# Optimization experiments

Hardware: AMD Instinct MI355X
Metric: run time of the kernel (lower is better)

The kernel has to match this reference:

```python
import jax, jax.numpy as jnp
import numpy as np

T_LATENCY = 2  # refractory latency (timesteps), from init_kwargs
FS_SCALE = 10.0  # FastSigmoid surrogate scale


@jax.custom_vjp
def fast_sigmoid_spike(u):
    return (u > 0).astype(u.dtype)

def _fs_fwd(u):
    return fast_sigmoid_spike(u), u

def _fs_bwd(u, g):
    return (g / (FS_SCALE * jnp.abs(u) + 1.0) ** 2,)

fast_sigmoid_spike.defvjp(_fs_fwd, _fs_bwd)


def setup_inputs() -> dict:
    key = jax.random.key(0)
    k1, k2, k3, k4 = jax.random.split(key, 4)
    B, N, T = 64, 1024, 512
    x = jax.random.normal(k1, (B, N, T), dtype=jnp.float32)
    beta = jax.random.uniform(k2, (N,), jnp.float32, 0.3, 0.95)   # leak
    p = jax.random.uniform(k3, (N,), jnp.float32, 0.5, 0.95)      # adaptation decay
    b = jax.random.uniform(k4, (N,), jnp.float32, 0.5, 1.5)       # adaptation strength
    return {"x": x, "beta": beta, "p": p, "b": b}


def reference(x, beta, p, b):
    # clamped effective params (matches torch @property accessors)
    beta_c = jnp.clip(beta, 0.001, 0.999)
    p_c = jnp.clip(jnp.abs(p), 0.0, 0.999)
    b_c = jnp.clip(jnp.abs(b), 0.001, 1.0)

    B, N, T = x.shape
    xt = jnp.moveaxis(x, 2, 0)  # [T, B, N]

    def step(carry, x_t):
        mem, spikes, refac, a, v_th = carry
        # spike-triggered refractory reset, then mask input during refractory window
        refac = jnp.where(spikes > 0, 0.0, refac)
        ic = jnp.where(refac < T_LATENCY, 0.0, x_t)
        refac = refac + 1.0
        # leaky integration
        new_mem = mem * beta_c + ic
        s = fast_sigmoid_spike(new_mem - v_th)
        # reset-by-subtraction-to-zero with detached spikes (detach_spike_grad=True)
        mem = new_mem * (1.0 - jax.lax.stop_gradient(s))
        # adaptive threshold
        a = p_c * a + s
        v_th = 1.0 + b_c * a
        return (mem, s, refac, a, v_th), s

    z = jnp.zeros((B, N), x.dtype)
    init = (z, z, jnp.full((B, N), float(T_LATENCY), x.dtype), z,
            jnp.ones((B, N), x.dtype))
    _, spikes_seq = jax.lax.scan(step, init, xt)  # [T, B, N]
    return jnp.moveaxis(spikes_seq, 0, 2)  # [B, N, T]
```

## Files before the change

### kernel.cpp

```cpp
#include <hip/hip_runtime.h>

#pragma clang fp contract(off)

#define ROWS    64
#define T_LEN   512
#define CHUNK   64
#define NCHUNK  (T_LEN / CHUNK)
#define STRIDE  (CHUNK + 1)
#define NV      16
#define NPARAM  1024

typedef float f4_nt __attribute__((ext_vector_type(4)));

#define BARRIER() asm volatile("s_waitcnt lgkmcnt(0)\n\ts_barrier" ::: "memory")

__global__ __launch_bounds__(192) void snn_fwd(
    const float* __restrict__ x,
    const float* __restrict__ beta,
    const float* __restrict__ p,
    const float* __restrict__ bparam,
    float* __restrict__ out)
{
    __shared__ float inbuf[2][ROWS * STRIDE];
    __shared__ float outbuf[ROWS * STRIDE];

    const int tid     = threadIdx.x;
    const int wid     = tid >> 6;
    const int lane    = tid & 63;
    const int rowBase = blockIdx.x * ROWS;

    const float4* __restrict__ xv = (const float4*)x;
    float4* __restrict__ ov       = (float4*)out;

    const int t16 = lane & 15;
    const int r4  = lane >> 4;
    const int gq  = (rowBase + r4) * (T_LEN / 4) + t16;
    const int lf  = r4 * STRIDE + t16 * 4;

    float mem = 0.0f, refac = 2.0f, a = 0.0f, vth = 1.0f, ps = 0.0f;
    float beta_c = 0.f, p_c = 0.f, b_c = 0.f;
    const int cb = lane * STRIDE;

    if (wid == 0) {
        const int n = (rowBase + lane) & (NPARAM - 1);
        beta_c = fminf(fmaxf(beta[n], 0.001f), 0.999f);
        p_c    = fminf(fabsf(p[n]), 0.999f);
        b_c    = fminf(fmaxf(fabsf(bparam[n]), 0.001f), 1.0f);
    }

    auto step = [&](float xt) -> float {
        refac = (ps > 0.0f) ? 0.0f : refac;
        const float ic = (refac < 2.0f) ? 0.0f : xt;
        refac += 1.0f;
        const float nm   = __fadd_rn(__fmul_rn(mem, beta_c), ic);
        const float diff = __fsub_rn(nm, vth);
        const float s    = (diff > 0.0f) ? 1.0f : 0.0f;
        mem = (diff > 0.0f) ? 0.0f : nm;
        a   = __fadd_rn(__fmul_rn(p_c, a), s);
        vth = __fadd_rn(1.0f, __fmul_rn(b_c, a));
        ps  = s;
        return s;
    };

    float4 ld[NV];

    auto loadChunk = [&](int k) {
        const int base = gq + k * NV;
        #pragma unroll
        for (int it = 0; it < NV; ++it)
            ld[it] = xv[base + it * 4 * (T_LEN / 4)];
    };
    auto stage = [&](int buf) {
        #pragma unroll
        for (int it = 0; it < NV; ++it) {
            const int o = lf + it * 4 * STRIDE;
            inbuf[buf][o + 0] = ld[it].x;
            inbuf[buf][o + 1] = ld[it].y;
            inbuf[buf][o + 2] = ld[it].z;
            inbuf[buf][o + 3] = ld[it].w;
        }
    };
    auto drain = [&](int k) {
        const int base = gq + k * NV;
        #pragma unroll
        for (int it = 0; it < NV; ++it) {
            const int o = lf + it * 4 * STRIDE;
            float4 sv;
            sv.x = outbuf[o + 0];
            sv.y = outbuf[o + 1];
            sv.z = outbuf[o + 2];
            sv.w = outbuf[o + 3];
            __builtin_nontemporal_store(
                *reinterpret_cast<f4_nt*>(&sv),
                reinterpret_cast<f4_nt*>(&ov[base + it * 4 * (T_LEN / 4)]));
        }
    };

    if (wid == 1) {
        loadChunk(0);
        stage(0);
        loadChunk(1);
    }
    BARRIER();

    #pragma unroll 1
    for (int k = 0; k < NCHUNK; ++k) {
        const int cur = k & 1;
        float sv[CHUNK];
        if (wid == 0) {
            #pragma unroll
            for (int t = 0; t < CHUNK; ++t)
                sv[t] = step(inbuf[cur][cb + t]);
        } else if (wid == 1) {
            if (k + 1 < NCHUNK) stage(cur ^ 1);
            if (k + 2 < NCHUNK) loadChunk(k + 2);
        } else {
            if (k > 0) drain(k - 1);
        }
        BARRIER();
        if (wid == 0) {
            #pragma unroll
            for (int t = 0; t < CHUNK; ++t)
                outbuf[cb + t] = sv[t];
        }
        BARRIER();
    }
    if (wid == 2) drain(NCHUNK - 1);
}

extern "C" void kernel_launch(void* const* d_in, const int* in_sizes, int n_in,
                              void* d_out, int out_size, void* d_ws, size_t ws_size,
                              hipStream_t stream) {
    const float* x    = (const float*)d_in[0];
    const float* beta = (const float*)d_in[1];
    const float* p    = (const float*)d_in[2];
    const float* b    = (const float*)d_in[3];
    float* out        = (float*)d_out;

    const int BN = 64 * 1024;
    snn_fwd<<<dim3(BN / ROWS), dim3(192), 0, stream>>>(x, beta, p, b, out);
}
```

Baseline: 241.5 us.

## Compute spikes in place in double-buffered XOR-swizzled LDS with two I/O waves

The compute wave now writes spikes back over its input slot instead of into a separate output buffer, which removes the second barrier per chunk. The chunk doubles to 128 timesteps, halving the number of loop iterations and barriers. Padded rows are replaced by an XOR swizzle to avoid LDS bank conflicts. Both helper waves now split the load, stage and drain work for 32 rows each, and each drains the previous results before restaging the buffer. The cost is higher register pressure, since 128 steps are fully unrolled and each lane now holds the full NV float4 loads, and occupancy may drop with 64 KB of LDS per block.

```diff
diff --git a/kernel.cpp b/kernel.cpp
--- a/kernel.cpp
+++ b/kernel.cpp
@@ -4,11 +4,11 @@
 
 #define ROWS    64
 #define T_LEN   512
-#define CHUNK   64
+#define CHUNK   128
 #define NCHUNK  (T_LEN / CHUNK)
-#define STRIDE  (CHUNK + 1)
 #define NV      16
 #define NPARAM  1024
+#define BUF_FLOATS (ROWS * CHUNK)
 
 typedef float f4_nt __attribute__((ext_vector_type(4)));
 
@@ -21,8 +21,7 @@
     const float* __restrict__ bparam,
     float* __restrict__ out)
 {
-    __shared__ float inbuf[2][ROWS * STRIDE];
-    __shared__ float outbuf[ROWS * STRIDE];
+    __shared__ float smem[2][BUF_FLOATS];
 
     const int tid     = threadIdx.x;
     const int wid     = tid >> 6;
@@ -32,14 +31,15 @@
     const float4* __restrict__ xv = (const float4*)x;
     float4* __restrict__ ov       = (float4*)out;
 
-    const int t16 = lane & 15;
-    const int r4  = lane >> 4;
-    const int gq  = (rowBase + r4) * (T_LEN / 4) + t16;
-    const int lf  = r4 * STRIDE + t16 * 4;
+    const int t32 = lane & 31;
+    const int r2  = lane >> 5;
+    const int rw  = (wid > 0 ? (wid - 1) * 32 : 0) + r2;
+    const int gq  = (rowBase + rw) * (T_LEN / 4) + t32;
 
     float mem = 0.0f, refac = 2.0f, a = 0.0f, vth = 1.0f, ps = 0.0f;
     float beta_c = 0.f, p_c = 0.f, b_c = 0.f;
-    const int cb = lane * STRIDE;
+    const int crow = lane * CHUNK;
+    const int cxm  = lane & 31;
 
     if (wid == 0) {
         const int n = (rowBase + lane) & (NPARAM - 1);
@@ -65,67 +65,70 @@
     float4 ld[NV];
 
     auto loadChunk = [&](int k) {
-        const int base = gq + k * NV;
+        const int base = gq + k * (CHUNK / 4);
         #pragma unroll
         for (int it = 0; it < NV; ++it)
-            ld[it] = xv[base + it * 4 * (T_LEN / 4)];
+            ld[it] = xv[base + it * 2 * (T_LEN / 4)];
     };
-    auto stage = [&](int buf) {
+    auto stage = [&](float* buf) {
         #pragma unroll
         for (int it = 0; it < NV; ++it) {
-            const int o = lf + it * 4 * STRIDE;
-            inbuf[buf][o + 0] = ld[it].x;
-            inbuf[buf][o + 1] = ld[it].y;
-            inbuf[buf][o + 2] = ld[it].z;
-            inbuf[buf][o + 3] = ld[it].w;
+            const int row = rw + 2 * it;
+            const int o   = row * CHUNK;
+            const int xm  = row & 31;
+            const int c0  = t32 * 4;
+            buf[o + ((c0 + 0) ^ xm)] = ld[it].x;
+            buf[o + ((c0 + 1) ^ xm)] = ld[it].y;
+            buf[o + ((c0 + 2) ^ xm)] = ld[it].z;
+            buf[o + ((c0 + 3) ^ xm)] = ld[it].w;
         }
     };
-    auto drain = [&](int k) {
-        const int base = gq + k * NV;
+    auto drain = [&](const float* buf, int k) {
+        const int base = gq + k * (CHUNK / 4);
         #pragma unroll
         for (int it = 0; it < NV; ++it) {
-            const int o = lf + it * 4 * STRIDE;
+            const int row = rw + 2 * it;
+            const int o   = row * CHUNK;
+            const int xm  = row & 31;
+            const int c0  = t32 * 4;
             float4 sv;
-            sv.x = outbuf[o + 0];
-            sv.y = outbuf[o + 1];
-            sv.z = outbuf[o + 2];
-            sv.w = outbuf[o + 3];
+            sv.x = buf[o + ((c0 + 0) ^ xm)];
+            sv.y = buf[o + ((c0 + 1) ^ xm)];
+            sv.z = buf[o + ((c0 + 2) ^ xm)];
+            sv.w = buf[o + ((c0 + 3) ^ xm)];
             __builtin_nontemporal_store(
                 *reinterpret_cast<f4_nt*>(&sv),
-                reinterpret_cast<f4_nt*>(&ov[base + it * 4 * (T_LEN / 4)]));
+                reinterpret_cast<f4_nt*>(&ov[base + it * 2 * (T_LEN / 4)]));
         }
     };
 
-    if (wid == 1) {
+    if (wid != 0) {
         loadChunk(0);
-        stage(0);
+        stage(smem[0]);
         loadChunk(1);
     }
     BARRIER();
 
     #pragma unroll 1
     for (int k = 0; k < NCHUNK; ++k) {
-        const int cur = k & 1;
-        float sv[CHUNK];
+        float* A = smem[k & 1];
+        float* B = smem[(k & 1) ^ 1];
         if (wid == 0) {
             #pragma unroll
-            for (int t = 0; t < CHUNK; ++t)
-                sv[t] = step(inbuf[cur][cb + t]);
-        } else if (wid == 1) {
-            if (k + 1 < NCHUNK) stage(cur ^ 1);
+            for (int t = 0; t < CHUNK; ++t) {
+                const int idx = crow + (t ^ cxm);
+                const float s = step(A[idx]);
+                A[idx] = s;
+            }
+        } else {
+            if (k > 0) drain(B, k - 1);
+            asm volatile("s_waitcnt lgkmcnt(0)" ::: "memory");
+            if (k + 1 < NCHUNK) stage(B);
             if (k + 2 < NCHUNK) loadChunk(k + 2);
-        } else {
-            if (k > 0) drain(k - 1);
-        }
-        BARRIER();
-        if (wid == 0) {
-            #pragma unroll
-            for (int t = 0; t < CHUNK; ++t)
-                outbuf[cb + t] = sv[t];
         }
         BARRIER();
     }
-    if (wid == 2) drain(NCHUNK - 1);
+    if (wid != 0) drain(smem[(NCHUNK - 1) & 1], NCHUNK - 1);
 }
 
 extern "C" void kernel_launch(void* const* d_in, const int* in_sizes, int n_in,
```

Result: slower. 259.1 us (+7.3%).

## Skew chunk schedule across 8-lane groups with wavefront phases

Applied to the files above, without the earlier changes.

Replaces the uniform chunk loop with a skewed wavefront schedule. Each 8-lane group of the compute wave handles chunk k minus its group index, and the load, stage and drain waves work on matching per-row-group chunk offsets across NCHUNK+7 phases. The aim appears to be spreading global memory traffic across several chunks at once instead of bursting on one. The cost is that the serial compute wave now runs 15 phases instead of 8, and inactive lanes still occupy the SIMD, which lengthens the critical path.

```diff
diff --git a/kernel.cpp b/kernel.cpp
--- a/kernel.cpp
+++ b/kernel.cpp
@@ -6,6 +6,7 @@
 #define T_LEN   512
 #define CHUNK   64
 #define NCHUNK  (T_LEN / CHUNK)
+#define NPHASE  (NCHUNK + 7)
 #define STRIDE  (CHUNK + 1)
 #define NV      16
 #define NPARAM  1024
@@ -40,6 +41,7 @@
     float mem = 0.0f, refac = 2.0f, a = 0.0f, vth = 1.0f, ps = 0.0f;
     float beta_c = 0.f, p_c = 0.f, b_c = 0.f;
     const int cb = lane * STRIDE;
+    const int cq = lane >> 3;
 
     if (wid == 0) {
         const int n = (rowBase + lane) & (NPARAM - 1);
@@ -64,68 +66,79 @@
 
     float4 ld[NV];
 
-    auto loadChunk = [&](int k) {
-        const int base = gq + k * NV;
-        #pragma unroll
-        for (int it = 0; it < NV; ++it)
-            ld[it] = xv[base + it * 4 * (T_LEN / 4)];
-    };
-    auto stage = [&](int buf) {
+    auto loadPhase = [&](int kp) {
         #pragma unroll
         for (int it = 0; it < NV; ++it) {
-            const int o = lf + it * 4 * STRIDE;
-            inbuf[buf][o + 0] = ld[it].x;
-            inbuf[buf][o + 1] = ld[it].y;
-            inbuf[buf][o + 2] = ld[it].z;
-            inbuf[buf][o + 3] = ld[it].w;
+            const int c = kp + 2 - (it >> 1);
+            if (0 <= c && c < NCHUNK)
+                ld[it] = xv[gq + c * NV + it * 4 * (T_LEN / 4)];
         }
     };
-    auto drain = [&](int k) {
-        const int base = gq + k * NV;
+    auto stagePhase = [&](int kp, int buf) {
         #pragma unroll
         for (int it = 0; it < NV; ++it) {
-            const int o = lf + it * 4 * STRIDE;
-            float4 sv;
-            sv.x = outbuf[o + 0];
-            sv.y = outbuf[o + 1];
-            sv.z = outbuf[o + 2];
-            sv.w = outbuf[o + 3];
-            __builtin_nontemporal_store(
-                *reinterpret_cast<f4_nt*>(&sv),
-                reinterpret_cast<f4_nt*>(&ov[base + it * 4 * (T_LEN / 4)]));
+            const int c = kp + 1 - (it >> 1);
+            if (0 <= c && c < NCHUNK) {
+                const int o = lf + it * 4 * STRIDE;
+                inbuf[buf][o + 0] = ld[it].x;
+                inbuf[buf][o + 1] = ld[it].y;
+                inbuf[buf][o + 2] = ld[it].z;
+                inbuf[buf][o + 3] = ld[it].w;
+            }
+        }
+    };
+    auto drainPhase = [&](int kp) {
+        #pragma unroll
+        for (int it = 0; it < NV; ++it) {
+            const int c = kp - 1 - (it >> 1);
+            if (0 <= c && c < NCHUNK) {
+                const int o = lf + it * 4 * STRIDE;
+                float4 sv;
+                sv.x = outbuf[o + 0];
+                sv.y = outbuf[o + 1];
+                sv.z = outbuf[o + 2];
+                sv.w = outbuf[o + 3];
+                __builtin_nontemporal_store(
+                    *reinterpret_cast<f4_nt*>(&sv),
+                    reinterpret_cast<f4_nt*>(&ov[gq + c * NV + it * 4 * (T_LEN / 4)]));
+            }
         }
     };
 
     if (wid == 1) {
-        loadChunk(0);
-        stage(0);
-        loadChunk(1);
+        loadPhase(-2);
+        stagePhase(-1, 0);
+        loadPhase(-1);
     }
     BARRIER();
 
     #pragma unroll 1
-    for (int k = 0; k < NCHUNK; ++k) {
+    for (int k = 0; k < NPHASE; ++k) {
         const int cur = k & 1;
         float sv[CHUNK];
+        const int  cc  = k - cq;
+        const bool act = (wid == 0) & (cc >= 0) & (cc < NCHUNK);
         if (wid == 0) {
-            #pragma unroll
-            for (int t = 0; t < CHUNK; ++t)
-                sv[t] = step(inbuf[cur][cb + t]);
+            if (act) {
+                #pragma unroll
+                for (int t = 0; t < CHUNK; ++t)
+                    sv[t] = step(inbuf[cur][cb + t]);
+            }
         } else if (wid == 1) {
-            if (k + 1 < NCHUNK) stage(cur ^ 1);
-            if (k + 2 < NCHUNK) loadChunk(k + 2);
+            stagePhase(k, cur ^ 1);
+            loadPhase(k);
         } else {
-            if (k > 0) drain(k - 1);
+            drainPhase(k);
         }
         BARRIER();
-        if (wid == 0) {
+        if (act) {
             #pragma unroll
             for (int t = 0; t < CHUNK; ++t)
                 outbuf[cb + t] = sv[t];
         }
         BARRIER();
     }
-    if (wid == 2) drain(NCHUNK - 1);
+    if (wid == 2) drainPhase(NPHASE);
 }
 
 extern "C" void kernel_launch(void* const* d_in, const int* in_sizes, int n_in,
```

Result: slower. 290.9 us (+20.4%).

## Use direct global-to-LDS loads with triple buffering and bit-packed spike output

Applied to the files above, without the earlier changes.

Replaces the register-staged input path with global_load_lds direct-to-LDS copies into a three-slot XOR-swizzled buffer, so the loader wave no longer round-trips data through VGPRs and ds_write. The compute wave reads float4 vectors and packs the 64 spikes per row into two 32-bit masks instead of writing 64 floats to LDS. The drain wave then expands those bits back to floats for the output stores. This cuts LDS traffic and register pressure, but the added swizzle and vmcnt bookkeeping are correctness risks.

```diff
diff --git a/kernel.cpp b/kernel.cpp
--- a/kernel.cpp
+++ b/kernel.cpp
@@ -6,13 +6,18 @@
 #define T_LEN   512
 #define CHUNK   64
 #define NCHUNK  (T_LEN / CHUNK)
-#define STRIDE  (CHUNK + 1)
 #define NV      16
+#define BUFW    (ROWS * CHUNK)
 #define NPARAM  1024
 
 typedef float f4_nt __attribute__((ext_vector_type(4)));
 
 #define BARRIER() asm volatile("s_waitcnt lgkmcnt(0)\n\ts_barrier" ::: "memory")
+
+#define GLOAD16(gp, lp)                                                \
+    __builtin_amdgcn_global_load_lds(                                  \
+        (const __attribute__((address_space(1))) void*)(gp),           \
+        (__attribute__((address_space(3))) void*)(lp), 16, 0, 0)
 
 __global__ __launch_bounds__(192) void snn_fwd(
     const float* __restrict__ x,
@@ -21,8 +26,8 @@
     const float* __restrict__ bparam,
     float* __restrict__ out)
 {
-    __shared__ float inbuf[2][ROWS * STRIDE];
-    __shared__ float outbuf[ROWS * STRIDE];
+    __shared__ __align__(16) float inbuf[3][BUFW];
+    __shared__ __align__(16) unsigned int outw[ROWS][4];
 
     const int tid     = threadIdx.x;
     const int wid     = tid >> 6;
@@ -34,12 +39,14 @@
 
     const int t16 = lane & 15;
     const int r4  = lane >> 4;
-    const int gq  = (rowBase + r4) * (T_LEN / 4) + t16;
-    const int lf  = r4 * STRIDE + t16 * 4;
+    const int gEven = (rowBase + r4) * (T_LEN / 4) + (t16 ^ r4);
+    const int gOdd  = gEven ^ 4;
+    const int gq = (rowBase + r4) * (T_LEN / 4) + t16;
 
     float mem = 0.0f, refac = 2.0f, a = 0.0f, vth = 1.0f, ps = 0.0f;
     float beta_c = 0.f, p_c = 0.f, b_c = 0.f;
-    const int cb = lane * STRIDE;
+    const int swl   = (lane & 3) | (((lane >> 2) & 1) << 2);
+    const int cbase = lane * NV;
 
     if (wid == 0) {
         const int n = (rowBase + lane) & (NPARAM - 1);
@@ -48,82 +55,97 @@
         b_c    = fminf(fmaxf(fabsf(bparam[n]), 0.001f), 1.0f);
     }
 
-    auto step = [&](float xt) -> float {
+    unsigned int b0 = 0, b1 = 0;
+
+    auto step = [&](float xt, unsigned int msk, unsigned int& bw) {
         refac = (ps > 0.0f) ? 0.0f : refac;
         const float ic = (refac < 2.0f) ? 0.0f : xt;
         refac += 1.0f;
         const float nm   = __fadd_rn(__fmul_rn(mem, beta_c), ic);
         const float diff = __fsub_rn(nm, vth);
-        const float s    = (diff > 0.0f) ? 1.0f : 0.0f;
-        mem = (diff > 0.0f) ? 0.0f : nm;
+        const bool  sp   = diff > 0.0f;
+        const float s    = sp ? 1.0f : 0.0f;
+        bw |= sp ? msk : 0u;
+        mem = sp ? 0.0f : nm;
         a   = __fadd_rn(__fmul_rn(p_c, a), s);
         vth = __fadd_rn(1.0f, __fmul_rn(b_c, a));
         ps  = s;
-        return s;
     };
 
-    float4 ld[NV];
-
-    auto loadChunk = [&](int k) {
-        const int base = gq + k * NV;
-        #pragma unroll
-        for (int it = 0; it < NV; ++it)
-            ld[it] = xv[base + it * 4 * (T_LEN / 4)];
-    };
-    auto stage = [&](int buf) {
+    auto issue = [&](int c, int buf) {
+        float* lb = &inbuf[buf][0];
         #pragma unroll
         for (int it = 0; it < NV; ++it) {
-            const int o = lf + it * 4 * STRIDE;
-            inbuf[buf][o + 0] = ld[it].x;
-            inbuf[buf][o + 1] = ld[it].y;
-            inbuf[buf][o + 2] = ld[it].z;
-            inbuf[buf][o + 3] = ld[it].w;
+            const int gidx = ((it & 1) ? gOdd : gEven)
+                           + it * 4 * (T_LEN / 4) + c * NV;
+            GLOAD16(&xv[gidx], lb + it * 256);
         }
     };
-    auto drain = [&](int k) {
-        const int base = gq + k * NV;
+
+    auto drain = [&](int c) {
         #pragma unroll
         for (int it = 0; it < NV; ++it) {
-            const int o = lf + it * 4 * STRIDE;
+            const int row = r4 + 4 * it;
+            const uint2 bits = *(const uint2*)&outw[row][0];
+            const unsigned int w = (t16 & 8) ? bits.y : bits.x;
+            const int sh = (t16 & 7) * 4;
             float4 sv;
-            sv.x = outbuf[o + 0];
-            sv.y = outbuf[o + 1];
-            sv.z = outbuf[o + 2];
-            sv.w = outbuf[o + 3];
+            sv.x = (float)((w >> (sh + 0)) & 1u);
+            sv.y = (float)((w >> (sh + 1)) & 1u);
+            sv.z = (float)((w >> (sh + 2)) & 1u);
+            sv.w = (float)((w >> (sh + 3)) & 1u);
             __builtin_nontemporal_store(
                 *reinterpret_cast<f4_nt*>(&sv),
-                reinterpret_cast<f4_nt*>(&ov[base + it * 4 * (T_LEN / 4)]));
+                reinterpret_cast<f4_nt*>(&ov[gq + c * NV + it * 4 * (T_LEN / 4)]));
         }
     };
 
     if (wid == 1) {
-        loadChunk(0);
-        stage(0);
-        loadChunk(1);
+        issue(0, 0);
+        issue(1, 1);
+        asm volatile("s_waitcnt vmcnt(16)");
     }
     BARRIER();
 
+    int km3 = 0;
     #pragma unroll 1
     for (int k = 0; k < NCHUNK; ++k) {
-        const int cur = k & 1;
-        float sv[CHUNK];
         if (wid == 0) {
+            b0 = 0; b1 = 0;
+            const float4* ib = (const float4*)inbuf[km3];
             #pragma unroll
-            for (int t = 0; t < CHUNK; ++t)
-                sv[t] = step(inbuf[cur][cb + t]);
-        } else if (wid == 1) {
-            if (k + 1 < NCHUNK) stage(cur ^ 1);
-            if (k + 2 < NCHUNK) loadChunk(k + 2);
-        } else {
+            for (int g = 0; g < NV; ++g) {
+                const float4 v = ib[cbase + (g ^ swl)];
+                const int t = 4 * g;
+                if (t < 32) {
+                    step(v.x, 1u << (t + 0), b0);
+                    step(v.y, 1u << (t + 1), b0);
+                    step(v.z, 1u << (t + 2), b0);
+                    step(v.w, 1u << (t + 3), b0);
+                } else {
+                    step(v.x, 1u << (t - 32), b1);
+                    step(v.y, 1u << (t - 31), b1);
+                    step(v.z, 1u << (t - 30), b1);
+                    step(v.w, 1u << (t - 29), b1);
+                }
+            }
+        } else if (wid == 2) {
             if (k > 0) drain(k - 1);
         }
         BARRIER();
         if (wid == 0) {
-            #pragma unroll
-            for (int t = 0; t < CHUNK; ++t)
-                outbuf[cb + t] = sv[t];
+            *(uint2*)&outw[lane][0] = make_uint2(b0, b1);
+        } else if (wid == 1) {
+            int nb = km3 + 2; if (nb >= 3) nb -= 3;
+            if (k + 2 < NCHUNK) {
+                issue(k + 2, nb);
+                asm volatile("s_waitcnt vmcnt(16)");
+            } else {
+                asm volatile("s_waitcnt vmcnt(0)");
+            }
         }
         BARRIER();
+        ++km3; if (km3 == 3) km3 = 0;
     }
     if (wid == 2) drain(NCHUNK - 1);
 }
```

Measured after the change: 247.9 us. +2.6%, slower.
